# Optimization experiments

Measured on AMD Instinct MI355X. Metric: run time of the kernel, lower is better.

## Reference

```python
import jax, jax.numpy as jnp
import numpy as np

BATCH, N_BEADS, BEAD_SIZE, N_ATOMS = 32, 16384, 16, 100000
INV_SQRT2 = 0.7071067811865476  # e3nn 'uuu' 1o x 1o -> 1e (irrep_normalization='none') cross-product scale


def _mask_arrays():
    # Deterministic bead->atom mask: bead h places count_h = (h % 16) + 1 atoms.
    counts = np.arange(N_BEADS) % BEAD_SIZE + 1
    mask = np.arange(BEAD_SIZE)[None, :] < counts[:, None]  # (n_beads, bead_size)
    slot_idx = np.nonzero(mask.ravel())[0].astype(np.int32)  # flat positions of True entries, (M,)
    bead_idx = np.repeat(np.arange(N_BEADS), counts).astype(np.int32)  # bead id per placed atom, (M,)
    return slot_idx, bead_idx


def setup_inputs() -> dict:
    slot_idx, bead_idx = _mask_arrays()
    M = slot_idx.shape[0]  # 139264
    rng = np.random.default_rng(0)
    atom_idx = rng.integers(0, N_ATOMS, size=M).astype(np.int32)  # bead2atom_idcs flattened over beads
    key = jax.random.key(0)
    kP, k1, k2, kw, ka, ks = jax.random.split(key, 6)
    return {
        'P': jax.random.normal(kP, (BATCH, N_BEADS, 3), jnp.float32),
        'p1': jax.random.normal(k1, (BATCH, N_BEADS, 3), jnp.float32),
        'p2': jax.random.normal(k2, (BATCH, N_BEADS, 3), jnp.float32),
        'weights': jax.random.normal(kw, (3, N_BEADS, BEAD_SIZE), jnp.float32),
        'angles_polar': jax.random.normal(ka, (M, 1), jnp.float32),
        'scaling': jax.random.normal(ks, (N_ATOMS, 1), jnp.float32),
        'slot_idx': jnp.asarray(slot_idx),
        'atom_idx': jnp.asarray(atom_idx),
        'bead_idx': jnp.asarray(bead_idx),
    }


def _q_mult(q1, q2):
    w1, x1, y1, z1 = jnp.moveaxis(q1, -1, 0)
    w2, x2, y2, z2 = jnp.moveaxis(q2, -1, 0)
    w = w1 * w2 - x1 * x2 - y1 * y2 - z1 * z2
    x = w1 * x2 + x1 * w2 + y1 * z2 - z1 * y2
    y = w1 * y2 + y1 * w2 + z1 * x2 - x1 * z2
    z = w1 * z2 + z1 * w2 + x1 * y2 - y1 * x2
    return jnp.stack((w, x, y, z), -1)


def _qv_mult(q, v):
    q2 = jnp.concatenate([jnp.zeros(v.shape[:-1] + (1,), v.dtype), v], -1)
    q_conj = q * jnp.asarray([1.0, -1.0, -1.0, -1.0], q.dtype)
    return _q_mult(_q_mult(q, q2), q_conj)[..., 1:]


def reference(P, p1, p2, weights, angles_polar, scaling, slot_idx, atom_idx, bead_idx):
    B = P.shape[0]
    # per-bead cross product (e3nn TensorProduct 'uuu' path)
    p12 = jnp.cross(p1, p2) * jnp.asarray(INV_SQRT2, p1.dtype)
    stacked = jnp.stack([p1, p2, p12], axis=1)                      # (B, 3, H, 3)
    rot = jnp.einsum('bihk,ihl->bhlk', stacked, weights)            # (B, H, L, 3)
    rot = rot / jnp.linalg.norm(rot, axis=-1, keepdims=True)
    rot_flat = rot.reshape(B, N_BEADS * BEAD_SIZE, 3)[:, slot_idx]  # (B, M, 3) gather via mask
    # quaternions: real = cos(theta), imag = sin(theta) * axis
    cos_a = jnp.cos(angles_polar)                                   # (M, 1)
    sin_a = jnp.sin(angles_polar)
    q = jnp.concatenate([jnp.broadcast_to(cos_a, (B,) + cos_a.shape), sin_a[None] * rot_flat], -1)  # (B, M, 4)
    v = p1[:, bead_idx]                                             # (B, M, 3) repeat_interleave by counts
    v_rot = _qv_mult(q, v)                                          # (B, M, 3)
    recon = scaling[atom_idx][None] * v_rot + P[:, bead_idx]        # (B, M, 3)
    out = jnp.zeros((B, N_ATOMS, 3), P.dtype).at[:, atom_idx].add(recon)  # scatter-add (overlaps accumulate)
    return out, rot_flat.reshape(-1, 3)
```

## Files before the change

### kernel.cpp

```cpp
#include <hip/hip_runtime.h>
#include <math.h>

#define BATCH   32
#define N_BEADS 16384
#define BEAD_SIZE 16
#define N_ATOMS 100000
#define INV_SQRT2 0.70710678118654752440f
#define SCAN_BLK 256

__global__ void __launch_bounds__(256)
zero_kernel(int* __restrict__ p, int n)
{
    int i = blockIdx.x * 256 + threadIdx.x;
    if (i < n) p[i] = 0;
}

__global__ void __launch_bounds__(256)
countrec_kernel(const int* __restrict__ atom_idx,
                const int* __restrict__ slot_idx,
                const float* __restrict__ W,
                int* __restrict__ counts,
                float4* __restrict__ rec1, int M)
{
    int m = blockIdx.x * blockDim.x + threadIdx.x;
    if (m >= M) return;
    atomicAdd(&counts[atom_idx[m]], 1);
    int slot = slot_idx[m];
    int h = slot >> 4, l = slot & 15;
    float w0 = W[(0 * N_BEADS + h) * BEAD_SIZE + l];
    float w1 = W[(1 * N_BEADS + h) * BEAD_SIZE + l];
    float w2 = W[(2 * N_BEADS + h) * BEAD_SIZE + l];
    rec1[m] = make_float4(__int_as_float(slot), w0, w1, w2);
}

__global__ void __launch_bounds__(SCAN_BLK)
scan1_kernel(const int* __restrict__ counts, int* __restrict__ off,
             int* __restrict__ bsum, int n)
{
    __shared__ int s[SCAN_BLK];
    int i = blockIdx.x * SCAN_BLK + threadIdx.x;
    int c = (i < n) ? counts[i] : 0;
    s[threadIdx.x] = c;
    __syncthreads();
    int v = c;
    for (int d = 1; d < SCAN_BLK; d <<= 1) {
        int t = (threadIdx.x >= d) ? s[threadIdx.x - d] : 0;
        __syncthreads();
        v += t;
        s[threadIdx.x] = v;
        __syncthreads();
    }
    if (i < n) off[i] = v - c;
    if (threadIdx.x == SCAN_BLK - 1) bsum[blockIdx.x] = v;
}

__global__ void __launch_bounds__(256)
scan3_kernel(int* __restrict__ off, const int* __restrict__ bsum,
             const int* __restrict__ counts,
             int* __restrict__ cursor2, float4* __restrict__ rec_a, int n)
{
    __shared__ int red[256];
    int j = blockIdx.x;
    int partial = 0;
    for (int i = threadIdx.x; i < j; i += 256) partial += bsum[i];
    red[threadIdx.x] = partial;
    __syncthreads();
    for (int d = 128; d > 0; d >>= 1) {
        if ((int)threadIdx.x < d) red[threadIdx.x] += red[threadIdx.x + d];
        __syncthreads();
    }
    int bpref = red[0];
    int i = j * 256 + threadIdx.x;
    if (i >= n) return;
    int o = off[i] + bpref;
    off[i] = o;
    cursor2[i] = 0;
    rec_a[i] = make_float4(__int_as_float(counts[i]), __int_as_float(o),
                           0.f, 0.f);
}

__global__ void __launch_bounds__(256)
fill2_kernel(const int* __restrict__ atom_idx, const int* __restrict__ off,
             const float* __restrict__ ang, const float* __restrict__ scal,
             int* __restrict__ cursor2, int* __restrict__ csr_m,
             float4* __restrict__ recM2, int M)
{
    int m = blockIdx.x * blockDim.x + threadIdx.x;
    if (m >= M) return;
    int a = atom_idx[m];
    int k = atomicAdd(&cursor2[a], 1);
    csr_m[off[a] + k] = m;
    float sa, ca;
    __sincosf(ang[m], &sa, &ca);
    recM2[m] = make_float4(2.f * ca * sa, 2.f * sa * sa, scal[a], 0.f);
}

__global__ void __launch_bounds__(256)
mcontrib_kernel(const float4* __restrict__ rec1,
                const float4* __restrict__ recM2,
                const float* __restrict__ p1,
                const float* __restrict__ p2,
                const float* __restrict__ P,
                float* __restrict__ out_rot,
                float* __restrict__ cM,
                int M)
{
    int bg = blockIdx.y;
    int mbase = blockIdx.x * 256;
    int m = mbase + threadIdx.x;
    int b0 = bg * 4;
    bool act = m < M;
    int mc = act ? m : (M - 1);

    float4 r1 = rec1[mc];
    float4 r2 = recM2[mc];
    int h = __float_as_int(r1.x) >> 4;
    float A = r2.x, Bc = r2.y, s = r2.z;
    size_t hoff = (size_t)h * 3;

    __shared__ float sbuf[768];
    int nm = M - mbase; if (nm > 256) nm = 256;
    int nf = nm * 3;
    int nf4 = nf >> 2;
    int done = nf4 << 2;
    int rem = nf - done;

#pragma unroll
    for (int i = 0; i < 4; ++i) {
        int b = b0 + i;
        const size_t bb = (size_t)b * N_BEADS * 3;
        const float* p1p = p1 + bb + hoff;
        const float* p2p = p2 + bb + hoff;
        const float* Pp  = P  + bb + hoff;
        float a1x = p1p[0], a1y = p1p[1], a1z = p1p[2];
        float a2x = p2p[0], a2y = p2p[1], a2z = p2p[2];

        float cxx = (a1y * a2z - a1z * a2y) * INV_SQRT2;
        float cyy = (a1z * a2x - a1x * a2z) * INV_SQRT2;
        float czz = (a1x * a2y - a1y * a2x) * INV_SQRT2;
        float rx = r1.y * a1x + r1.z * a2x + r1.w * cxx;
        float ry = r1.y * a1y + r1.z * a2y + r1.w * cyy;
        float rz = r1.y * a1z + r1.z * a2z + r1.w * czz;
        float inv = rsqrtf(rx * rx + ry * ry + rz * rz);
        rx *= inv; ry *= inv; rz *= inv;

        __syncthreads();
        sbuf[threadIdx.x * 3 + 0] = rx;
        sbuf[threadIdx.x * 3 + 1] = ry;
        sbuf[threadIdx.x * 3 + 2] = rz;
        __syncthreads();
        {
            size_t base = ((size_t)b * M + mbase) * 3;
            float4* dst = (float4*)(out_rot + base);
            if (((base & 3) == 0)) {
                if ((int)threadIdx.x < nf4)
                    dst[threadIdx.x] = ((const float4*)sbuf)[threadIdx.x];
                if ((int)threadIdx.x < rem)
                    out_rot[base + done + threadIdx.x] = sbuf[done + threadIdx.x];
            } else if (act) {
                out_rot[base + threadIdx.x * 3 + 0] = rx;
                out_rot[base + threadIdx.x * 3 + 1] = ry;
                out_rot[base + threadIdx.x * 3 + 2] = rz;
            }
        }

        float ux = ry * a1z - rz * a1y;
        float uy = rz * a1x - rx * a1z;
        float uz = rx * a1y - ry * a1x;
        float wx = ry * uz - rz * uy;
        float wy = rz * ux - rx * uz;
        float wz = rx * uy - ry * ux;
        float ox = s * (a1x + A * ux + Bc * wx) + Pp[0];
        float oy = s * (a1y + A * uy + Bc * wy) + Pp[1];
        float oz = s * (a1z + A * uz + Bc * wz) + Pp[2];

        __syncthreads();
        sbuf[threadIdx.x * 3 + 0] = ox;
        sbuf[threadIdx.x * 3 + 1] = oy;
        sbuf[threadIdx.x * 3 + 2] = oz;
        __syncthreads();
        {
            size_t base = ((size_t)b * M + mbase) * 3;
            float4* dst = (float4*)(cM + base);
            if (((base & 3) == 0)) {
                if ((int)threadIdx.x < nf4)
                    dst[threadIdx.x] = ((const float4*)sbuf)[threadIdx.x];
                if ((int)threadIdx.x < rem)
                    cM[base + done + threadIdx.x] = sbuf[done + threadIdx.x];
            } else if (act) {
                cM[base + threadIdx.x * 3 + 0] = ox;
                cM[base + threadIdx.x * 3 + 1] = oy;
                cM[base + threadIdx.x * 3 + 2] = oz;
            }
        }
    }
}

__global__ void __launch_bounds__(256)
sum2_kernel(const float4* __restrict__ rec_a,
            const int* __restrict__ csr_m,
            const float* __restrict__ cM,
            float* __restrict__ out_atoms, int M, int abps)
{
    int beta = blockIdx.x;
    int xcd  = beta & 7;
    int j    = beta >> 3;
    int round = j / abps;
    int ablk  = j - round * abps;
    int b = xcd + 8 * round;
    int abase = ablk * 256;
    int a = abase + threadIdx.x;

    float ax = 0.f, ay = 0.f, az = 0.f;
    if (a < N_ATOMS) {
        float4 ra = rec_a[a];
        int cnt = __float_as_int(ra.x);
        int o   = __float_as_int(ra.y);
        const float* cb = cM + (size_t)b * M * 3;
        for (int k = 0; k < cnt; ++k) {
            int m = csr_m[o + k];
            const float* cp = cb + (size_t)m * 3;
            ax += cp[0]; ay += cp[1]; az += cp[2];
        }
    }
    __shared__ float sbuf[768];
    sbuf[threadIdx.x * 3 + 0] = ax;
    sbuf[threadIdx.x * 3 + 1] = ay;
    sbuf[threadIdx.x * 3 + 2] = az;
    __syncthreads();

    int na = N_ATOMS - abase; if (na > 256) na = 256;
    int nf = na * 3;
    size_t base = ((size_t)b * N_ATOMS + abase) * 3;
    int nf4 = nf >> 2;
    float4* dst = (float4*)(out_atoms + base);
    if ((int)threadIdx.x < nf4)
        dst[threadIdx.x] = ((const float4*)sbuf)[threadIdx.x];
    int done = nf4 << 2;
    int rem = nf - done;
    if ((int)threadIdx.x < rem)
        out_atoms[base + done + threadIdx.x] = sbuf[done + threadIdx.x];
}

__global__ void __launch_bounds__(256)
backmap_fallback(const float* __restrict__ P, const float* __restrict__ p1,
                 const float* __restrict__ p2, const float* __restrict__ W,
                 const float* __restrict__ ang, const float* __restrict__ scal,
                 const int* __restrict__ slot_idx, const int* __restrict__ atom_idx,
                 float* __restrict__ out_atoms, float* __restrict__ out_rot, int M)
{
    int t = blockIdx.x * blockDim.x + threadIdx.x;
    if (t >= BATCH * M) return;
    int b = t / M; int m = t - b * M;
    int slot = slot_idx[m]; int h = slot >> 4; int l = slot & 15;
    int atom = atom_idx[m];
    const float* p1p = p1 + ((size_t)b * N_BEADS + h) * 3;
    const float* p2p = p2 + ((size_t)b * N_BEADS + h) * 3;
    float a1x = p1p[0], a1y = p1p[1], a1z = p1p[2];
    float a2x = p2p[0], a2y = p2p[1], a2z = p2p[2];
    float cx = (a1y * a2z - a1z * a2y) * INV_SQRT2;
    float cy = (a1z * a2x - a1x * a2z) * INV_SQRT2;
    float cz = (a1x * a2y - a1y * a2x) * INV_SQRT2;
    float w0 = W[(0 * N_BEADS + h) * BEAD_SIZE + l];
    float w1 = W[(1 * N_BEADS + h) * BEAD_SIZE + l];
    float w2 = W[(2 * N_BEADS + h) * BEAD_SIZE + l];
    float rx = w0 * a1x + w1 * a2x + w2 * cx;
    float ry = w0 * a1y + w1 * a2y + w2 * cy;
    float rz = w0 * a1z + w1 * a2z + w2 * cz;
    float inv = rsqrtf(rx * rx + ry * ry + rz * rz);
    rx *= inv; ry *= inv; rz *= inv;
    float* ro = out_rot + (size_t)t * 3;
    ro[0] = rx; ro[1] = ry; ro[2] = rz;
    float sa, ca; __sincosf(ang[m], &sa, &ca);
    float A = 2.f * ca * sa, Bc = 2.f * sa * sa;
    float ux = ry * a1z - rz * a1y;
    float uy = rz * a1x - rx * a1z;
    float uz = rx * a1y - ry * a1x;
    float wx = ry * uz - rz * uy;
    float wy = rz * ux - rx * uz;
    float wz = rx * uy - ry * ux;
    float s = scal[atom];
    const float* Pp = P + ((size_t)b * N_BEADS + h) * 3;
    float* op = out_atoms + ((size_t)b * N_ATOMS + atom) * 3;
    atomicAdd(op + 0, s * (a1x + A * ux + Bc * wx) + Pp[0]);
    atomicAdd(op + 1, s * (a1y + A * uy + Bc * wy) + Pp[1]);
    atomicAdd(op + 2, s * (a1z + A * uz + Bc * wz) + Pp[2]);
}

extern "C" void kernel_launch(void* const* d_in, const int* in_sizes, int n_in,
                              void* d_out, int out_size, void* d_ws, size_t ws_size,
                              hipStream_t stream) {
    const float* P    = (const float*)d_in[0];
    const float* p1   = (const float*)d_in[1];
    const float* p2   = (const float*)d_in[2];
    const float* W    = (const float*)d_in[3];
    const float* ang  = (const float*)d_in[4];
    const float* scal = (const float*)d_in[5];
    const int* slot_idx = (const int*)d_in[6];
    const int* atom_idx = (const int*)d_in[7];

    int M = in_sizes[6];
    float* out_atoms = (float*)d_out;
    float* out_rot   = out_atoms + (size_t)BATCH * N_ATOMS * 3;

    int nblk   = (N_ATOMS + SCAN_BLK - 1) / SCAN_BLK;
    int nchunk = (M + 255) / 256;

    size_t intpre = (size_t)N_ATOMS * 4 * 3 + 512 * 4;
    size_t need   = intpre + (size_t)M * 16 * 2 + (size_t)N_ATOMS * 16
                  + (size_t)M * 4 + (size_t)BATCH * M * 3 * 4;

    if (ws_size >= need) {
        int* counts  = (int*)d_ws;
        int* off     = counts + N_ATOMS;
        int* cursor2 = off + N_ATOMS;
        int* bsum    = cursor2 + N_ATOMS;
        float4* rec1  = (float4*)((char*)d_ws + intpre);
        float4* recM2 = rec1 + M;
        float4* rec_a = recM2 + M;
        int*    csr_m = (int*)(rec_a + N_ATOMS);
        float*  cM    = (float*)(csr_m + M);

        zero_kernel<<<nblk, 256, 0, stream>>>(counts, N_ATOMS);
        countrec_kernel<<<nchunk, 256, 0, stream>>>(
            atom_idx, slot_idx, W, counts, rec1, M);
        scan1_kernel<<<nblk, SCAN_BLK, 0, stream>>>(counts, off, bsum, N_ATOMS);
        scan3_kernel<<<nblk, 256, 0, stream>>>(off, bsum, counts,
                                               cursor2, rec_a, N_ATOMS);
        fill2_kernel<<<nchunk, 256, 0, stream>>>(
            atom_idx, off, ang, scal, cursor2, csr_m, recM2, M);

        dim3 gm(nchunk, 8);
        mcontrib_kernel<<<gm, 256, 0, stream>>>(
            rec1, recM2, p1, p2, P, out_rot, cM, M);

        int abps = (N_ATOMS + 255) / 256;
        sum2_kernel<<<abps * BATCH, 256, 0, stream>>>(
            rec_a, csr_m, cM, out_atoms, M, abps);
        return;
    }

    hipMemsetAsync(out_atoms, 0, (size_t)BATCH * N_ATOMS * 3 * sizeof(float), stream);
    int total = BATCH * M;
    backmap_fallback<<<(total + 255) / 256, 256, 0, stream>>>(
        P, p1, p2, W, ang, scal, slot_idx, atom_idx,
        out_atoms, out_rot, M);
}
```

Before: 98.27 us.

## Store per-atom contributions as fp16 in CSR order to drop indirection

The per-(batch, placement) contributions are now stored as packed half-precision triples at their CSR position, written directly by the contribution kernel. The sum kernel can then read contiguously without the csr_m indirection. The grid axes are also swapped so that batch groups are adjacent for the same chunk. This cuts intermediate traffic and the gather indirection, but it adds fp16 rounding error to the accumulated outputs and makes the cM writes scattered.

New measurement: 113.6 us. 15.6% more time.

```diff
diff --git a/kernel.cpp b/kernel.cpp
--- a/kernel.cpp
+++ b/kernel.cpp
@@ -1,4 +1,5 @@
 #include <hip/hip_runtime.h>
+#include <hip/hip_fp16.h>
 #include <math.h>
 
 #define BATCH   32
@@ -82,14 +83,14 @@
 __global__ void __launch_bounds__(256)
 fill2_kernel(const int* __restrict__ atom_idx, const int* __restrict__ off,
              const float* __restrict__ ang, const float* __restrict__ scal,
-             int* __restrict__ cursor2, int* __restrict__ csr_m,
+             int* __restrict__ cursor2, int* __restrict__ csr_pos,
              float4* __restrict__ recM2, int M)
 {
     int m = blockIdx.x * blockDim.x + threadIdx.x;
     if (m >= M) return;
     int a = atom_idx[m];
     int k = atomicAdd(&cursor2[a], 1);
-    csr_m[off[a] + k] = m;
+    csr_pos[m] = off[a] + k;
     float sa, ca;
     __sincosf(ang[m], &sa, &ca);
     recM2[m] = make_float4(2.f * ca * sa, 2.f * sa * sa, scal[a], 0.f);
@@ -98,15 +99,16 @@
 __global__ void __launch_bounds__(256)
 mcontrib_kernel(const float4* __restrict__ rec1,
                 const float4* __restrict__ recM2,
+                const int*  __restrict__ csr_pos,
                 const float* __restrict__ p1,
                 const float* __restrict__ p2,
                 const float* __restrict__ P,
                 float* __restrict__ out_rot,
-                float* __restrict__ cM,
+                uint2* __restrict__ cM16,
                 int M)
 {
-    int bg = blockIdx.y;
-    int mbase = blockIdx.x * 256;
+    int bg = blockIdx.x;
+    int mbase = blockIdx.y * 256;
     int m = mbase + threadIdx.x;
     int b0 = bg * 4;
     bool act = m < M;
@@ -114,6 +116,7 @@
 
     float4 r1 = rec1[mc];
     float4 r2 = recM2[mc];
+    int pos = csr_pos[mc];
     int h = __float_as_int(r1.x) >> 4;
     float A = r2.x, Bc = r2.y, s = r2.z;
     size_t hoff = (size_t)h * 3;
@@ -152,7 +155,7 @@
         {
             size_t base = ((size_t)b * M + mbase) * 3;
             float4* dst = (float4*)(out_rot + base);
-            if (((base & 3) == 0)) {
+            if ((base & 3) == 0) {
                 if ((int)threadIdx.x < nf4)
                     dst[threadIdx.x] = ((const float4*)sbuf)[threadIdx.x];
                 if ((int)threadIdx.x < rem)
@@ -174,32 +177,18 @@
         float oy = s * (a1y + A * uy + Bc * wy) + Pp[1];
         float oz = s * (a1z + A * uz + Bc * wz) + Pp[2];
 
-        __syncthreads();
-        sbuf[threadIdx.x * 3 + 0] = ox;
-        sbuf[threadIdx.x * 3 + 1] = oy;
-        sbuf[threadIdx.x * 3 + 2] = oz;
-        __syncthreads();
-        {
-            size_t base = ((size_t)b * M + mbase) * 3;
-            float4* dst = (float4*)(cM + base);
-            if (((base & 3) == 0)) {
-                if ((int)threadIdx.x < nf4)
-                    dst[threadIdx.x] = ((const float4*)sbuf)[threadIdx.x];
-                if ((int)threadIdx.x < rem)
-                    cM[base + done + threadIdx.x] = sbuf[done + threadIdx.x];
-            } else if (act) {
-                cM[base + threadIdx.x * 3 + 0] = ox;
-                cM[base + threadIdx.x * 3 + 1] = oy;
-                cM[base + threadIdx.x * 3 + 2] = oz;
-            }
+        if (act) {
+            union { struct { __half2 lo, hi; } h; uint2 u; } pk;
+            pk.h.lo = __floats2half2_rn(ox, oy);
+            pk.h.hi = __floats2half2_rn(oz, 0.f);
+            cM16[(size_t)b * M + pos] = pk.u;
         }
     }
 }
 
 __global__ void __launch_bounds__(256)
 sum2_kernel(const float4* __restrict__ rec_a,
-            const int* __restrict__ csr_m,
-            const float* __restrict__ cM,
+            const uint2* __restrict__ cM16,
             float* __restrict__ out_atoms, int M, int abps)
 {
     int beta = blockIdx.x;
@@ -216,11 +205,13 @@
         float4 ra = rec_a[a];
         int cnt = __float_as_int(ra.x);
         int o   = __float_as_int(ra.y);
-        const float* cb = cM + (size_t)b * M * 3;
+        const uint2* cb = cM16 + (size_t)b * M;
         for (int k = 0; k < cnt; ++k) {
-            int m = csr_m[o + k];
-            const float* cp = cb + (size_t)m * 3;
-            ax += cp[0]; ay += cp[1]; az += cp[2];
+            union { uint2 u; struct { __half2 lo, hi; } h; } pk;
+            pk.u = cb[o + k];
+            float2 xy = __half22float2(pk.h.lo);
+            float2 zp = __half22float2(pk.h.hi);
+            ax += xy.x; ay += xy.y; az += zp.x;
         }
     }
     __shared__ float sbuf[768];
@@ -308,18 +299,18 @@
 
     size_t intpre = (size_t)N_ATOMS * 4 * 3 + 512 * 4;
     size_t need   = intpre + (size_t)M * 16 * 2 + (size_t)N_ATOMS * 16
-                  + (size_t)M * 4 + (size_t)BATCH * M * 3 * 4;
+                  + (size_t)M * 4 + (size_t)BATCH * M * 8;
 
     if (ws_size >= need) {
         int* counts  = (int*)d_ws;
         int* off     = counts + N_ATOMS;
         int* cursor2 = off + N_ATOMS;
         int* bsum    = cursor2 + N_ATOMS;
-        float4* rec1  = (float4*)((char*)d_ws + intpre);
-        float4* recM2 = rec1 + M;
-        float4* rec_a = recM2 + M;
-        int*    csr_m = (int*)(rec_a + N_ATOMS);
-        float*  cM    = (float*)(csr_m + M);
+        float4* rec1   = (float4*)((char*)d_ws + intpre);
+        float4* recM2  = rec1 + M;
+        float4* rec_a  = recM2 + M;
+        int*    csr_pos = (int*)(rec_a + N_ATOMS);
+        uint2*  cM16   = (uint2*)(csr_pos + M);
 
         zero_kernel<<<nblk, 256, 0, stream>>>(counts, N_ATOMS);
         countrec_kernel<<<nchunk, 256, 0, stream>>>(
@@ -328,15 +319,15 @@
         scan3_kernel<<<nblk, 256, 0, stream>>>(off, bsum, counts,
                                                cursor2, rec_a, N_ATOMS);
         fill2_kernel<<<nchunk, 256, 0, stream>>>(
-            atom_idx, off, ang, scal, cursor2, csr_m, recM2, M);
-
-        dim3 gm(nchunk, 8);
+            atom_idx, off, ang, scal, cursor2, csr_pos, recM2, M);
+
+        dim3 gm(8, nchunk);
         mcontrib_kernel<<<gm, 256, 0, stream>>>(
-            rec1, recM2, p1, p2, P, out_rot, cM, M);
+            rec1, recM2, csr_pos, p1, p2, P, out_rot, cM16, M);
 
         int abps = (N_ATOMS + 255) / 256;
         sum2_kernel<<<abps * BATCH, 256, 0, stream>>>(
-            rec_a, csr_m, cM, out_atoms, M, abps);
+            rec_a, cM16, out_atoms, M, abps);
         return;
     }
 
```
